# Kernel tuning notes

Hardware: AMD Instinct MI355X
Metric: run time of the kernel (lower is better)

Reference implementation:

```python
import jax, jax.numpy as jnp
import numpy as np

VOCAB, EMB_DIM, HIDDEN, NUM_CLASSES = 100000, 128, 256, 20
B, S = 4096, 200


def setup_inputs() -> dict:
    key = jax.random.key(0)
    k1, k2, k3, k4, k5, k6, k7 = jax.random.split(key, 7)
    x = jax.random.randint(k1, (B, S), 0, VOCAB, dtype=jnp.int64)
    seq_lengths = jnp.maximum(jax.random.randint(k2, (B,), 0, S, dtype=jnp.int64), 1)
    emb = jax.random.normal(k3, (VOCAB, EMB_DIM), dtype=jnp.float32) * 0.02
    emb = emb.at[0].set(0.0)  # padding_idx=0
    W1 = jax.random.normal(k4, (EMB_DIM, HIDDEN), dtype=jnp.float32) * (1.0 / np.sqrt(EMB_DIM))
    b1 = jax.random.normal(k5, (HIDDEN,), dtype=jnp.float32) * 0.01
    W2 = jax.random.normal(k6, (HIDDEN, NUM_CLASSES), dtype=jnp.float32) * (1.0 / np.sqrt(HIDDEN))
    b2 = jax.random.normal(k7, (NUM_CLASSES,), dtype=jnp.float32) * 0.01
    return {"x": x, "seq_lengths": seq_lengths, "emb": emb, "W1": W1, "b1": b1, "W2": W2, "b2": b2}


def reference(x, seq_lengths, emb, W1, b1, W2, b2):
    # Embedding lookup: [B, S, D]
    e = emb[x]
    # Masked mean over first seq_lengths[i] positions (fused, no per-sample loop)
    mask = (jnp.arange(S)[None, :] < seq_lengths[:, None]).astype(e.dtype)  # [B, S]
    pooled = jnp.einsum('bsd,bs->bd', e, mask) / seq_lengths[:, None].astype(e.dtype)
    # MLP (dropout is identity in eval mode)
    hidden = jax.nn.relu(pooled @ W1 + b1)
    return hidden @ W2 + b2
```

## Files before the change

kernel.cpp:

```cpp
#include <hip/hip_runtime.h>
#include <hip/hip_bf16.h>

#define B 4096
#define S 200
#define EMB_DIM 128
#define HIDDEN 256
#define NUM_CLASSES 20

__global__ __launch_bounds__(256, 4) void fused_kernel(
    const int* __restrict__ x,
    const int* __restrict__ lens,
    const float* __restrict__ emb,
    const float* __restrict__ W1,
    const float* __restrict__ b1,
    const float* __restrict__ W2,
    const float* __restrict__ b2,
    float* __restrict__ out)
{
    __shared__ int    sidx[256];
    __shared__ float4 tmp[8][32];
    __shared__ float  P[EMB_DIM];
    __shared__ float  H[HIDDEN];
    __shared__ float  part[8][NUM_CLASSES];

    const int b = blockIdx.x;
    const int t = threadIdx.x;
    const int L = lens[b];

    {
        int v = 0;
        if (t < L) v = x[(long)b * S + t];
        sidx[t] = v;
    }
    __syncthreads();

    const int g = t >> 5;
    const int d = t & 31;

    const int Lpad  = (L + 63) & ~63;
    const int nIter = Lpad >> 6;

    float4 acc[8];
    #pragma unroll
    for (int j = 0; j < 8; ++j) acc[j] = make_float4(0.f, 0.f, 0.f, 0.f);

    int cur[8], nxt[8];
    #pragma unroll
    for (int j = 0; j < 8; ++j) cur[j] = sidx[g + 8 * j];

    for (int it = 0; it < nIter; ++it) {
        float4 v[8];
        #pragma unroll
        for (int j = 0; j < 8; ++j)
            v[j] = ((const float4*)(emb + (long)cur[j] * EMB_DIM))[d];

        const int nb = (it + 1) << 6;
        if (it + 1 < nIter) {
            #pragma unroll
            for (int j = 0; j < 8; ++j) nxt[j] = sidx[nb + g + 8 * j];
        }

        #pragma unroll
        for (int j = 0; j < 8; ++j) {
            acc[j].x += v[j].x; acc[j].y += v[j].y;
            acc[j].z += v[j].z; acc[j].w += v[j].w;
        }
        #pragma unroll
        for (int j = 0; j < 8; ++j) cur[j] = nxt[j];
    }

    #pragma unroll
    for (int j = 1; j < 8; ++j) {
        acc[0].x += acc[j].x; acc[0].y += acc[j].y;
        acc[0].z += acc[j].z; acc[0].w += acc[j].w;
    }
    tmp[g][d] = acc[0];
    __syncthreads();

    if (t < 32) {
        float4 s0 = tmp[0][t];
        #pragma unroll
        for (int gg = 1; gg < 8; ++gg) {
            const float4 v = tmp[gg][t];
            s0.x += v.x; s0.y += v.y; s0.z += v.z; s0.w += v.w;
        }
        const float inv = 1.0f / (float)L;
        s0.x *= inv; s0.y *= inv; s0.z *= inv; s0.w *= inv;
        ((float4*)P)[t] = s0;
    }
    __syncthreads();

    {
        float h0 = 0.f, h1 = 0.f, h2 = 0.f, h3 = 0.f;
        for (int k = 0; k < EMB_DIM; k += 4) {
            h0 += P[k]     * W1[(k)     * HIDDEN + t];
            h1 += P[k + 1] * W1[(k + 1) * HIDDEN + t];
            h2 += P[k + 2] * W1[(k + 2) * HIDDEN + t];
            h3 += P[k + 3] * W1[(k + 3) * HIDDEN + t];
        }
        H[t] = fmaxf(h0 + h1 + h2 + h3 + b1[t], 0.f);
    }
    __syncthreads();

    if (t < 8 * NUM_CLASSES) {
        const int j = t / NUM_CLASSES;
        const int c = t - j * NUM_CLASSES;
        const int k0 = j * 32;
        float a = 0.f;
        for (int k = k0; k < k0 + 32; ++k)
            a += H[k] * W2[k * NUM_CLASSES + c];
        part[j][c] = a;
    }
    __syncthreads();

    if (t < NUM_CLASSES) {
        float a = b2[t];
        #pragma unroll
        for (int j = 0; j < 8; ++j) a += part[j][t];
        out[(long)b * NUM_CLASSES + t] = a;
    }
}

extern "C" void kernel_launch(void* const* d_in, const int* in_sizes, int n_in,
                              void* d_out, int out_size, void* d_ws, size_t ws_size,
                              hipStream_t stream) {
    const int*   x    = (const int*)d_in[0];
    const int*   lens = (const int*)d_in[1];
    const float* emb  = (const float*)d_in[2];
    const float* W1   = (const float*)d_in[3];
    const float* b1   = (const float*)d_in[4];
    const float* W2   = (const float*)d_in[5];
    const float* b2   = (const float*)d_in[6];
    float*       out  = (float*)d_out;

    fused_kernel<<<B, 256, 0, stream>>>(x, lens, emb, W1, b1, W2, b2, out);
}
```

Baseline: 126.5 us.

## Gather bf16 embedding copy and process two batch rows per block

A new pre-pass kernel converts the whole fp32 embedding table to bf16 in workspace on every call. The fused kernel then gathers 16-byte bf16 chunks, halving the bytes per gathered row, and widens them back to fp32 for accumulation. Each block now handles two batch rows, so the W1 loads in the first MLP layer are shared between them. The trade-off is an extra full-table read and write each call, plus bf16 rounding error in the pooled embeddings.

```diff
diff --git a/kernel.cpp b/kernel.cpp
--- a/kernel.cpp
+++ b/kernel.cpp
@@ -6,118 +6,151 @@
 #define EMB_DIM 128
 #define HIDDEN 256
 #define NUM_CLASSES 20
+#define VOCAB 100000
+#define RB 2
 
-__global__ __launch_bounds__(256, 4) void fused_kernel(
+typedef __attribute__((ext_vector_type(8))) unsigned short ushort8;
+
+__device__ __forceinline__ unsigned short f2bf(float f) {
+    unsigned u = __float_as_uint(f);
+    unsigned r = u + 0x7fffu + ((u >> 16) & 1u);
+    return (unsigned short)(r >> 16);
+}
+
+__global__ __launch_bounds__(256) void convert_kernel(
+    const float* __restrict__ emb,
+    unsigned short* __restrict__ embh)
+{
+    const long i = ((long)blockIdx.x * 256 + threadIdx.x) * 8;
+    const float4 a = *(const float4*)(emb + i);
+    const float4 b = *(const float4*)(emb + i + 4);
+    ushort8 o;
+    o[0] = f2bf(a.x); o[1] = f2bf(a.y); o[2] = f2bf(a.z); o[3] = f2bf(a.w);
+    o[4] = f2bf(b.x); o[5] = f2bf(b.y); o[6] = f2bf(b.z); o[7] = f2bf(b.w);
+    *(ushort8*)(embh + i) = o;
+}
+
+__global__ __launch_bounds__(256) void fused_kernel(
     const int* __restrict__ x,
     const int* __restrict__ lens,
-    const float* __restrict__ emb,
+    const unsigned short* __restrict__ embh,
     const float* __restrict__ W1,
     const float* __restrict__ b1,
     const float* __restrict__ W2,
     const float* __restrict__ b2,
     float* __restrict__ out)
 {
-    __shared__ int    sidx[256];
-    __shared__ float4 tmp[8][32];
-    __shared__ float  P[EMB_DIM];
-    __shared__ float  H[HIDDEN];
-    __shared__ float  part[8][NUM_CLASSES];
+    __shared__ int   sidx[RB][256];
+    __shared__ float tmp[16][16][8];
+    __shared__ float P[RB][EMB_DIM];
+    __shared__ float H[RB][HIDDEN];
+    __shared__ float part[RB][4][NUM_CLASSES];
 
-    const int b = blockIdx.x;
-    const int t = threadIdx.x;
-    const int L = lens[b];
+    const int t  = threadIdx.x;
+    const int b0 = blockIdx.x * RB;
 
-    {
+    int Ls[RB];
+    #pragma unroll
+    for (int r = 0; r < RB; ++r) {
+        Ls[r] = lens[b0 + r];
         int v = 0;
-        if (t < L) v = x[(long)b * S + t];
-        sidx[t] = v;
+        if (t < Ls[r]) v = x[(long)(b0 + r) * S + t];
+        sidx[r][t] = v;
     }
     __syncthreads();
 
-    const int g = t >> 5;
-    const int d = t & 31;
+    const int g = t >> 4;
+    const int d = t & 15;
 
-    const int Lpad  = (L + 63) & ~63;
-    const int nIter = Lpad >> 6;
+    for (int r = 0; r < RB; ++r) {
+        const int L = Ls[r];
+        const int nIter = ((L + 63) & ~63) >> 6;
 
-    float4 acc[8];
-    #pragma unroll
-    for (int j = 0; j < 8; ++j) acc[j] = make_float4(0.f, 0.f, 0.f, 0.f);
+        float acc[4][8];
+        #pragma unroll
+        for (int j = 0; j < 4; ++j)
+            #pragma unroll
+            for (int f = 0; f < 8; ++f) acc[j][f] = 0.f;
 
-    int cur[8], nxt[8];
-    #pragma unroll
-    for (int j = 0; j < 8; ++j) cur[j] = sidx[g + 8 * j];
+        int cur[4], nxt[4];
+        #pragma unroll
+        for (int j = 0; j < 4; ++j) cur[j] = sidx[r][g + 16 * j];
 
-    for (int it = 0; it < nIter; ++it) {
-        float4 v[8];
-        #pragma unroll
-        for (int j = 0; j < 8; ++j)
-            v[j] = ((const float4*)(emb + (long)cur[j] * EMB_DIM))[d];
+        for (int it = 0; it < nIter; ++it) {
+            uint4 v[4];
+            #pragma unroll
+            for (int j = 0; j < 4; ++j)
+                v[j] = *(const uint4*)(embh + (long)cur[j] * EMB_DIM + d * 8);
 
-        const int nb = (it + 1) << 6;
-        if (it + 1 < nIter) {
+            if (it + 1 < nIter) {
+                const int nb = (it + 1) << 6;
+                #pragma unroll
+                for (int j = 0; j < 4; ++j) nxt[j] = sidx[r][nb + g + 16 * j];
+            }
+
             #pragma unroll
-            for (int j = 0; j < 8; ++j) nxt[j] = sidx[nb + g + 8 * j];
+            for (int j = 0; j < 4; ++j) {
+                const unsigned c0 = v[j].x, c1 = v[j].y, c2 = v[j].z, c3 = v[j].w;
+                acc[j][0] += __uint_as_float(c0 << 16);
+                acc[j][1] += __uint_as_float(c0 & 0xffff0000u);
+                acc[j][2] += __uint_as_float(c1 << 16);
+                acc[j][3] += __uint_as_float(c1 & 0xffff0000u);
+                acc[j][4] += __uint_as_float(c2 << 16);
+                acc[j][5] += __uint_as_float(c2 & 0xffff0000u);
+                acc[j][6] += __uint_as_float(c3 << 16);
+                acc[j][7] += __uint_as_float(c3 & 0xffff0000u);
+            }
+            #pragma unroll
+            for (int j = 0; j < 4; ++j) cur[j] = nxt[j];
         }
 
         #pragma unroll
-        for (int j = 0; j < 8; ++j) {
-            acc[j].x += v[j].x; acc[j].y += v[j].y;
-            acc[j].z += v[j].z; acc[j].w += v[j].w;
+        for (int f = 0; f < 8; ++f)
+            tmp[g][d][f] = acc[0][f] + acc[1][f] + acc[2][f] + acc[3][f];
+        __syncthreads();
+
+        if (t < EMB_DIM) {
+            float s = 0.f;
+            #pragma unroll
+            for (int gg = 0; gg < 16; ++gg) s += tmp[gg][t >> 3][t & 7];
+            P[r][t] = s / (float)L;
         }
-        #pragma unroll
-        for (int j = 0; j < 8; ++j) cur[j] = nxt[j];
+        __syncthreads();
     }
 
-    #pragma unroll
-    for (int j = 1; j < 8; ++j) {
-        acc[0].x += acc[j].x; acc[0].y += acc[j].y;
-        acc[0].z += acc[j].z; acc[0].w += acc[j].w;
-    }
-    tmp[g][d] = acc[0];
-    __syncthreads();
-
-    if (t < 32) {
-        float4 s0 = tmp[0][t];
-        #pragma unroll
-        for (int gg = 1; gg < 8; ++gg) {
-            const float4 v = tmp[gg][t];
-            s0.x += v.x; s0.y += v.y; s0.z += v.z; s0.w += v.w;
+    {
+        float h0a = 0.f, h0b = 0.f, h1a = 0.f, h1b = 0.f;
+        for (int k = 0; k < EMB_DIM; k += 2) {
+            const float wa = W1[(k)     * HIDDEN + t];
+            const float wb = W1[(k + 1) * HIDDEN + t];
+            h0a += P[0][k] * wa;  h0b += P[0][k + 1] * wb;
+            h1a += P[1][k] * wa;  h1b += P[1][k + 1] * wb;
         }
-        const float inv = 1.0f / (float)L;
-        s0.x *= inv; s0.y *= inv; s0.z *= inv; s0.w *= inv;
-        ((float4*)P)[t] = s0;
+        const float bb = b1[t];
+        H[0][t] = fmaxf(h0a + h0b + bb, 0.f);
+        H[1][t] = fmaxf(h1a + h1b + bb, 0.f);
     }
     __syncthreads();
 
-    {
-        float h0 = 0.f, h1 = 0.f, h2 = 0.f, h3 = 0.f;
-        for (int k = 0; k < EMB_DIM; k += 4) {
-            h0 += P[k]     * W1[(k)     * HIDDEN + t];
-            h1 += P[k + 1] * W1[(k + 1) * HIDDEN + t];
-            h2 += P[k + 2] * W1[(k + 2) * HIDDEN + t];
-            h3 += P[k + 3] * W1[(k + 3) * HIDDEN + t];
-        }
-        H[t] = fmaxf(h0 + h1 + h2 + h3 + b1[t], 0.f);
+    if (t < RB * 4 * NUM_CLASSES) {
+        const int r  = t / (4 * NUM_CLASSES);
+        const int u  = t - r * 4 * NUM_CLASSES;
+        const int j  = u / NUM_CLASSES;
+        const int c  = u - j * NUM_CLASSES;
+        const int k0 = j * 64;
+        float a = 0.f;
+        for (int k = k0; k < k0 + 64; ++k)
+            a += H[r][k] * W2[k * NUM_CLASSES + c];
+        part[r][j][c] = a;
     }
     __syncthreads();
 
-    if (t < 8 * NUM_CLASSES) {
-        const int j = t / NUM_CLASSES;
-        const int c = t - j * NUM_CLASSES;
-        const int k0 = j * 32;
-        float a = 0.f;
-        for (int k = k0; k < k0 + 32; ++k)
-            a += H[k] * W2[k * NUM_CLASSES + c];
-        part[j][c] = a;
-    }
-    __syncthreads();
-
-    if (t < NUM_CLASSES) {
-        float a = b2[t];
-        #pragma unroll
-        for (int j = 0; j < 8; ++j) a += part[j][t];
-        out[(long)b * NUM_CLASSES + t] = a;
+    if (t < RB * NUM_CLASSES) {
+        const int r = t / NUM_CLASSES;
+        const int c = t - r * NUM_CLASSES;
+        const float a = b2[c] + part[r][0][c] + part[r][1][c]
+                              + part[r][2][c] + part[r][3][c];
+        out[(long)(b0 + r) * NUM_CLASSES + c] = a;
     }
 }
 
@@ -133,5 +166,8 @@
     const float* b2   = (const float*)d_in[6];
     float*       out  = (float*)d_out;
 
-    fused_kernel<<<B, 256, 0, stream>>>(x, lens, emb, W1, b1, W2, b2, out);
+    unsigned short* embh = (unsigned short*)d_ws;
+
+    convert_kernel<<<(VOCAB * EMB_DIM) / (8 * 256), 256, 0, stream>>>(emb, embh);
+    fused_kernel<<<B / RB, 256, 0, stream>>>(x, lens, embh, W1, b1, W2, b2, out);
 }
```

Measured after the change: 125.0 us. Within noise of the previous version (-1.2%).
